# Kernel tuning notes

Hardware: AMD Instinct MI355X
Metric: run time of the kernel (lower is better)

Reference implementation:

```python
import jax, jax.numpy as jnp
import numpy as np

H = 1024
V = 5000
NUM_LAYERS = 2
B, T, U = 2, 128, 64


def setup_inputs() -> dict:
    key = jax.random.key(0)
    ks = jax.random.split(key, 16)
    s = 0.02
    inp = {
        "encoder_out": jax.random.normal(ks[0], (B, T, H), dtype=jnp.float32),
        "targets": jax.random.randint(ks[1], (B, U), 0, V),
        "embed": jax.random.normal(ks[2], (V, H), dtype=jnp.float32) * s,
        # stacked 2-layer LSTM params, PyTorch gate order (i, f, g, o)
        "lstm_Wih": jax.random.normal(ks[3], (NUM_LAYERS, 4 * H, H), dtype=jnp.float32) * s,
        "lstm_Whh": jax.random.normal(ks[4], (NUM_LAYERS, 4 * H, H), dtype=jnp.float32) * s,
        "lstm_bih": jnp.zeros((NUM_LAYERS, 4 * H), dtype=jnp.float32),
        "lstm_bhh": jnp.zeros((NUM_LAYERS, 4 * H), dtype=jnp.float32),
        "enc_W": jax.random.normal(ks[5], (H, H), dtype=jnp.float32) * s,
        "enc_b": jnp.zeros((H,), dtype=jnp.float32),
        "pred_W": jax.random.normal(ks[6], (H, H), dtype=jnp.float32) * s,
        "pred_b": jnp.zeros((H,), dtype=jnp.float32),
        "out_W": jax.random.normal(ks[7], (V + 1, H), dtype=jnp.float32) * s,
        "out_b": jnp.zeros((V + 1,), dtype=jnp.float32),
    }
    return inp


def _lstm_layer(x, Wih, Whh, bih, bhh):
    # x: [B, U, H] -> [B, U, H]; single LSTM layer, PyTorch gate order i,f,g,o
    b, u, h = x.shape
    bias = bih + bhh  # [4H]
    # precompute input projections for all timesteps: [U, B, 4H]
    xg = jnp.einsum('buh,gh->ubg', x, Wih) + bias

    def step(carry, xt):
        hprev, cprev = carry
        gates = xt + hprev @ Whh.T  # [B, 4H]
        i, f, g, o = jnp.split(gates, 4, axis=-1)
        i = jax.nn.sigmoid(i)
        f = jax.nn.sigmoid(f)
        g = jnp.tanh(g)
        o = jax.nn.sigmoid(o)
        c = f * cprev + i * g
        hnew = o * jnp.tanh(c)
        return (hnew, c), hnew

    init = (jnp.zeros((b, h), x.dtype), jnp.zeros((b, h), x.dtype))
    _, hs = jax.lax.scan(step, init, xg)  # hs: [U, B, H]
    return hs.transpose(1, 0, 2)


def reference(encoder_out, targets, embed, lstm_Wih, lstm_Whh, lstm_bih, lstm_bhh,
              enc_W, enc_b, pred_W, pred_b, out_W, out_b):
    # Prediction network: embedding + 2-layer LSTM (deterministic -> no dropout)
    x = embed[targets]  # [B, U, H]
    for l in range(NUM_LAYERS):
        x = _lstm_layer(x, lstm_Wih[l], lstm_Whh[l], lstm_bih[l], lstm_bhh[l])
    pred_out = x  # [B, U, H]

    # Joint network: proj + broadcast add over (T, U) + ReLU + output linear
    enc_p = jnp.einsum('bth,oh->bto', encoder_out, enc_W) + enc_b  # [B, T, H]
    prd_p = jnp.einsum('buh,oh->buo', pred_out, pred_W) + pred_b    # [B, U, H]
    joint = jax.nn.relu(enc_p[:, :, None, :] + prd_p[:, None, :, :])  # [B, T, U, H]
    logits = jnp.einsum('btuh,vh->btuv', joint, out_W) + out_b  # [B, T, U, V+1]
    return logits
```

## Files before the change

kernel.cpp:

```cpp
#include <hip/hip_runtime.h>
#include <hip/hip_bf16.h>

#define B_ 2
#define T_ 128
#define U_ 64
#define H_ 1024
#define NO_ 5001

typedef __attribute__((ext_vector_type(8))) short bf16x8;
typedef __attribute__((ext_vector_type(4))) float f32x4;
typedef __attribute__((ext_vector_type(4))) unsigned int uint4v;

__device__ __forceinline__ float bf2f(unsigned short s) {
  unsigned int u = ((unsigned int)s) << 16;
  float f; __builtin_memcpy(&f, &u, 4); return f;
}
__device__ __forceinline__ unsigned short f2bf(float f) {
  unsigned int u; __builtin_memcpy(&u, &f, 4);
  u = u + 0x7FFFu + ((u >> 16) & 1u);
  return (unsigned short)(u >> 16);
}
__device__ __forceinline__ float fsig(float x) {
  x = fminf(fmaxf(x, -30.f), 30.f);
  float e = __expf(-x);
  return __builtin_amdgcn_rcpf(1.f + e);
}
__device__ __forceinline__ float ftanh(float x) {
  x = fminf(fmaxf(x, -15.f), 15.f);
  float e = __expf(2.f * x);
  return (e - 1.f) * __builtin_amdgcn_rcpf(e + 1.f);
}

__device__ __forceinline__ void gload_lds16(const unsigned short* g, unsigned short* l) {
  __builtin_amdgcn_global_load_lds(
      (const __attribute__((address_space(1))) unsigned int*)g,
      (__attribute__((address_space(3))) unsigned int*)l,
      16, 0, 0);
}

#define R_OUTW 1280256
#define R_WIH  (R_OUTW + 2097152)
#define R_WHH  (R_WIH + 2097152)
#define R_ENCW (R_WHH + 262144)
#define R_PRDW (R_ENCW + 262144)
#define R_ENC  (R_PRDW + 65536)
#define R_BIAS (R_ENC + 1280)

__global__ void k_cvt_all(
    const float* __restrict__ outW, const float* __restrict__ Wih,
    const float* __restrict__ Whh,  const float* __restrict__ encW,
    const float* __restrict__ prdW, const float* __restrict__ enc,
    const float* __restrict__ outB,
    unsigned short* __restrict__ outW_bf, unsigned short* __restrict__ Wih_bf,
    unsigned short* __restrict__ Whh_bf,  unsigned short* __restrict__ encW_bf,
    unsigned short* __restrict__ prdW_bf, unsigned short* __restrict__ enc_bf,
    float* __restrict__ biasPad)
{
  int i = blockIdx.x * 256 + threadIdx.x;
  const float* src; unsigned short* dst; int off;
  if (i < R_OUTW)      { src = outW; dst = outW_bf; off = i; }
  else if (i < R_WIH)  { src = Wih;  dst = Wih_bf;  off = i - R_OUTW; }
  else if (i < R_WHH)  { src = Whh;  dst = Whh_bf;  off = i - R_WIH; }
  else if (i < R_ENCW) { src = encW; dst = encW_bf; off = i - R_WHH; }
  else if (i < R_PRDW) { src = prdW; dst = prdW_bf; off = i - R_ENCW; }
  else if (i < R_ENC)  { src = enc;  dst = enc_bf;  off = i - R_PRDW; }
  else {
    int e0 = (i - R_ENC) * 4;
    float4 v;
    v.x = (e0 + 0 < NO_) ? outB[e0 + 0] : 0.f;
    v.y = (e0 + 1 < NO_) ? outB[e0 + 1] : 0.f;
    v.z = (e0 + 2 < NO_) ? outB[e0 + 2] : 0.f;
    v.w = (e0 + 3 < NO_) ? outB[e0 + 3] : 0.f;
    *(float4*)&biasPad[e0] = v;
    return;
  }
  const float4 v = ((const float4*)src)[off];
  ushort4 o;
  o.x = f2bf(v.x); o.y = f2bf(v.y); o.z = f2bf(v.z); o.w = f2bf(v.w);
  ((ushort4*)dst)[off] = o;
}

__global__ void k_embed(const int* __restrict__ tg, const float* __restrict__ em,
                        unsigned short* __restrict__ x0) {
  int idx = blockIdx.x * 256 + threadIdx.x;
  int bu = idx >> 8;
  int kc = (idx & 255) << 2;
  int t = tg[bu];
  const float4 v = *(const float4*)&em[(long)t * H_ + kc];
  ushort4 o; o.x = f2bf(v.x); o.y = f2bf(v.y); o.z = f2bf(v.z); o.w = f2bf(v.w);
  *(ushort4*)&x0[bu * H_ + kc] = o;
}

__global__ __launch_bounds__(256) void gemm_bt(
    const unsigned short* __restrict__ A, const unsigned short* __restrict__ W,
    const float* __restrict__ b1, const float* __restrict__ b2,
    float* __restrict__ C, int M, int N, int K)
{
  __shared__ unsigned short As[128 * 32];
  __shared__ unsigned short Bs[128 * 32];
  const int tid = threadIdx.x;
  const int n0 = blockIdx.x * 128, m0 = blockIdx.y * 128;
  const int lane = tid & 63, w = tid >> 6;
  const int wr = (w >> 1) * 64, wc = (w & 1) * 64;
  const int lr = lane & 15, lk = (lane >> 4) * 8;
  f32x4 acc[4][4] = {};

  for (int k0 = 0; k0 < K; k0 += 32) {
#pragma unroll
    for (int s = 0; s < 2; ++s) {
      int idx = (w * 2 + s) * 64 + lane;
      int row = idx >> 2, c8 = (idx & 3) * 8;
      gload_lds16(&A[(long)(m0 + row) * K + k0 + c8], &As[(w * 2 + s) * 512]);
      gload_lds16(&W[(long)(n0 + row) * K + k0 + c8], &Bs[(w * 2 + s) * 512]);
    }
    __syncthreads();
    bf16x8 aF[4], bF[4];
#pragma unroll
    for (int i = 0; i < 4; ++i) {
      aF[i] = *(const bf16x8*)&As[(wr + i * 16 + lr) * 32 + lk];
      bF[i] = *(const bf16x8*)&Bs[(wc + i * 16 + lr) * 32 + lk];
    }
#pragma unroll
    for (int i = 0; i < 4; ++i)
#pragma unroll
      for (int j = 0; j < 4; ++j)
        acc[i][j] = __builtin_amdgcn_mfma_f32_16x16x32_bf16(aF[i], bF[j], acc[i][j], 0, 0, 0);
    __syncthreads();
  }

  const int lq = (lane >> 4) * 4;
#pragma unroll
  for (int j = 0; j < 4; ++j) {
    int col = n0 + wc + j * 16 + lr;
    if (col >= N) continue;
    float bb = 0.f;
    if (b1) bb += b1[col];
    if (b2) bb += b2[col];
#pragma unroll
    for (int i = 0; i < 4; ++i) {
      int rowg = m0 + wr + i * 16 + lq;
#pragma unroll
      for (int r = 0; r < 4; ++r)
        C[(long)(rowg + r) * N + col] = acc[i][j][r] + bb;
    }
  }
}

__global__ __launch_bounds__(256) void gemm_proj(
    const unsigned short* __restrict__ enc_bf, const unsigned short* __restrict__ x2_bf,
    const unsigned short* __restrict__ encW_bf, const unsigned short* __restrict__ prdW_bf,
    const float* __restrict__ encB, const float* __restrict__ prdB,
    float* __restrict__ ep, float* __restrict__ pp)
{
  __shared__ unsigned short As[128 * 32];
  __shared__ unsigned short Bs[128 * 32];
  const int tid = threadIdx.x;
  const unsigned short* A; const unsigned short* W; const float* b1; float* C;
  int m0;
  if (blockIdx.y < 2) { A = enc_bf; W = encW_bf; b1 = encB; C = ep; m0 = blockIdx.y * 128; }
  else                { A = x2_bf;  W = prdW_bf; b1 = prdB; C = pp; m0 = 0; }
  const int n0 = blockIdx.x * 128;
  const int K = H_, N = H_;
  const int lane = tid & 63, w = tid >> 6;
  const int wr = (w >> 1) * 64, wc = (w & 1) * 64;
  const int lr = lane & 15, lk = (lane >> 4) * 8;
  f32x4 acc[4][4] = {};

  for (int k0 = 0; k0 < K; k0 += 32) {
#pragma unroll
    for (int s = 0; s < 2; ++s) {
      int idx = (w * 2 + s) * 64 + lane;
      int row = idx >> 2, c8 = (idx & 3) * 8;
      gload_lds16(&A[(long)(m0 + row) * K + k0 + c8], &As[(w * 2 + s) * 512]);
      gload_lds16(&W[(long)(n0 + row) * K + k0 + c8], &Bs[(w * 2 + s) * 512]);
    }
    __syncthreads();
    bf16x8 aF[4], bF[4];
#pragma unroll
    for (int i = 0; i < 4; ++i) {
      aF[i] = *(const bf16x8*)&As[(wr + i * 16 + lr) * 32 + lk];
      bF[i] = *(const bf16x8*)&Bs[(wc + i * 16 + lr) * 32 + lk];
    }
#pragma unroll
    for (int i = 0; i < 4; ++i)
#pragma unroll
      for (int j = 0; j < 4; ++j)
        acc[i][j] = __builtin_amdgcn_mfma_f32_16x16x32_bf16(aF[i], bF[j], acc[i][j], 0, 0, 0);
    __syncthreads();
  }

  const int lq = (lane >> 4) * 4;
#pragma unroll
  for (int j = 0; j < 4; ++j) {
    int col = n0 + wc + j * 16 + lr;
    float bb = b1[col];
#pragma unroll
    for (int i = 0; i < 4; ++i) {
      int rowg = m0 + wr + i * 16 + lq;
#pragma unroll
      for (int r = 0; r < 4; ++r)
        C[(long)(rowg + r) * N + col] = acc[i][j][r] + bb;
    }
  }
}

#define STAGE_A(kt2, kh, rb) \
  gload_lds16(aSrc[rb] + (kt2) * 64 + (kh) * 32, \
              &As_f[((((kt2) & 1) * 2 + (kh)) * 8192) + ((rb) * 128 + wv * 16) * 32])
#define STAGE_B(kt2, kh, rb) \
  gload_lds16(bSrc[rb] + (kt2) * 64 + (kh) * 32, \
              &Bs_f[((((kt2) & 1) * 2 + (kh)) * 8192) + ((rb) * 128 + wv * 16) * 32])

__global__ __launch_bounds__(512, 1) void gemm_logits(
    const unsigned short* __restrict__ A, const unsigned short* __restrict__ W,
    const float* __restrict__ biasPad, float* __restrict__ C, int M, int N, int K)
{
  __shared__ __align__(16) unsigned short lds_all[65536];
  unsigned short* As_f = lds_all;
  unsigned short* Bs_f = lds_all + 32768;
  const int tid = threadIdx.x;
  const int lane = tid & 63, wv = tid >> 6;
  const int wm = wv >> 2, wn = wv & 3;
  int swzb = (blockIdx.x & 7) * 160 + (blockIdx.x >> 3);
  const int n0 = (swzb >> 6) * 256;
  const int m0 = (swzb & 63) * 256;
  const int NT = K / 64;

  const unsigned short* aSrc[2];
  const unsigned short* bSrc[2];
#pragma unroll
  for (int rb = 0; rb < 2; ++rb) {
    int rl = rb * 128 + (tid >> 2);
    int c2s = (tid & 3) ^ ((rl >> 1) & 3);
    aSrc[rb] = A + (long)(m0 + rl) * K + c2s * 8;
    bSrc[rb] = W + (long)(n0 + rl) * K + c2s * 8;
  }
  int aOff[8], bOff[4];
#pragma unroll
  for (int i = 0; i < 8; ++i) {
    int r = wm * 128 + i * 16 + (lane & 15);
    aOff[i] = r * 32 + (((lane >> 4) ^ ((r >> 1) & 3)) * 8);
  }
#pragma unroll
  for (int j = 0; j < 4; ++j) {
    int r = wn * 64 + j * 16 + (lane & 15);
    bOff[j] = r * 32 + (((lane >> 4) ^ ((r >> 1) & 3)) * 8);
  }

  f32x4 acc[8][4] = {};

  STAGE_A(0, 0, 0); STAGE_A(0, 0, 1); STAGE_B(0, 0, 0); STAGE_B(0, 0, 1);
  STAGE_A(0, 1, 0); STAGE_A(0, 1, 1); STAGE_B(0, 1, 0); STAGE_B(0, 1, 1);

  for (int kt = 0; kt < NT; ++kt) {
    const int b = kt & 1;
    asm volatile("s_waitcnt vmcnt(4)" ::: "memory");
    __builtin_amdgcn_s_barrier();
    __builtin_amdgcn_sched_barrier(0);
    {
      const int base = (b * 2 + 0) * 8192;
      bf16x8 aF[8], bF[4];
#pragma unroll
      for (int i = 0; i < 8; ++i) aF[i] = *(const bf16x8*)&As_f[base + aOff[i]];
#pragma unroll
      for (int j = 0; j < 4; ++j) bF[j] = *(const bf16x8*)&Bs_f[base + bOff[j]];
      if (kt + 1 < NT) {
        STAGE_A(kt + 1, 0, 0); STAGE_A(kt + 1, 0, 1);
        STAGE_B(kt + 1, 0, 0); STAGE_B(kt + 1, 0, 1);
        STAGE_A(kt + 1, 1, 0); STAGE_A(kt + 1, 1, 1);
      }
      __builtin_amdgcn_s_setprio(1);
#pragma unroll
      for (int i = 0; i < 8; ++i)
#pragma unroll
        for (int j = 0; j < 4; ++j)
          acc[i][j] = __builtin_amdgcn_mfma_f32_16x16x32_bf16(aF[i], bF[j], acc[i][j], 0, 0, 0);
      __builtin_amdgcn_s_setprio(0);
    }
    if (kt + 1 < NT) { asm volatile("s_waitcnt vmcnt(6)" ::: "memory"); }
    else             { asm volatile("s_waitcnt vmcnt(0)" ::: "memory"); }
    __builtin_amdgcn_s_barrier();
    __builtin_amdgcn_sched_barrier(0);
    {
      const int base = (b * 2 + 1) * 8192;
      bf16x8 aF[8], bF[4];
#pragma unroll
      for (int i = 0; i < 8; ++i) aF[i] = *(const bf16x8*)&As_f[base + aOff[i]];
#pragma unroll
      for (int j = 0; j < 4; ++j) bF[j] = *(const bf16x8*)&Bs_f[base + bOff[j]];
      if (kt + 1 < NT) { STAGE_B(kt + 1, 1, 0); STAGE_B(kt + 1, 1, 1); }
      __builtin_amdgcn_s_setprio(1);
#pragma unroll
      for (int i = 0; i < 8; ++i)
#pragma unroll
        for (int j = 0; j < 4; ++j)
          acc[i][j] = __builtin_amdgcn_mfma_f32_16x16x32_bf16(aF[i], bF[j], acc[i][j], 0, 0, 0);
      __builtin_amdgcn_s_setprio(0);
    }
  }

  float* eb = (float*)lds_all;
  const int lq = (lane >> 4) * 4;
  float bv4[4];
#pragma unroll
  for (int j = 0; j < 4; ++j) bv4[j] = biasPad[n0 + wn * 64 + j * 16 + (lane & 15)];

#pragma unroll
  for (int cp = 0; cp < 4; ++cp) {
    __syncthreads();
#pragma unroll
    for (int ii = 0; ii < 2; ++ii) {
      int rbase = wm * 32 + ii * 16 + lq;
#pragma unroll
      for (int j = 0; j < 4; ++j) {
        int col = wn * 64 + j * 16 + (lane & 15);
#pragma unroll
        for (int r = 0; r < 4; ++r)
          eb[(rbase + r) * 261 + col] = acc[cp * 2 + ii][j][r] + bv4[j];
      }
    }
    __syncthreads();
    {
      int rl = tid >> 3, ci = tid & 7;
      long grow = (long)m0 + (rl >> 5) * 128 + cp * 32 + (rl & 31);
      float* crow = C + grow * N + n0;
      const float* er = &eb[rl * 261];
#pragma unroll
      for (int k = 0; k < 8; ++k) {
        int col = ci * 4 + k * 32;
        float4 v = *(const float4*)&er[col];
        int gc = n0 + col;
        if (gc + 4 <= N) {
          *(float4*)&crow[col] = v;
        } else if (gc < N) {
          float tmp[4] = {v.x, v.y, v.z, v.w};
#pragma unroll
          for (int e = 0; e < 4; ++e)
            if (gc + e < N) crow[col + e] = tmp[e];
        }
      }
    }
  }
}

__global__ __launch_bounds__(256, 1) void lstm_fused3(
    const float* __restrict__ xg0,
    const unsigned short* __restrict__ Whh0,
    const unsigned short* __restrict__ Whh1,
    const unsigned short* __restrict__ Wih1,
    const float* __restrict__ bih1, const float* __restrict__ bhh1,
    unsigned short* __restrict__ x2_bf,
    float* __restrict__ hbuf0,
    float* __restrict__ hbuf1,
    float* __restrict__ xbuf,
    float* __restrict__ xgbuf,
    int*   __restrict__ flagsx)
{
  __shared__ float hs[2][H_];
  __shared__ float xgs[128][64];
  __shared__ float part[2][4][64][2];
  __shared__ float bias2s[64];

  const int tid = threadIdx.x;
  const int grp = blockIdx.x >> 6;
  const int bid = blockIdx.x & 63;
  const int w = tid >> 6, l = tid & 63;
  const int g = l >> 4, q = l & 15;
  const int row = g * 1024 + bid * 16 + q;
  const int kb = w * 256;

#define DOT_BODY(WREG, SRC)                                                              \
  _Pragma("unroll")                                                                      \
  for (int it = 0; it < 32; ++it) {                                                      \
    bf16x8 wv = WREG[it];                                                                \
    float4 h0a = *(const float4*)&SRC[0][kb + it * 8];                                   \
    float4 h0b = *(const float4*)&SRC[0][kb + it * 8 + 4];                               \
    float4 h1a = *(const float4*)&SRC[1][kb + it * 8];                                   \
    float4 h1b = *(const float4*)&SRC[1][kb + it * 8 + 4];                               \
    a00 += bf2f((unsigned short)wv[0]) * h0a.x + bf2f((unsigned short)wv[4]) * h0b.x;    \
    a01 += bf2f((unsigned short)wv[1]) * h0a.y + bf2f((unsigned short)wv[5]) * h0b.y;    \
    a02 += bf2f((unsigned short)wv[2]) * h0a.z + bf2f((unsigned short)wv[6]) * h0b.z;    \
    a03 += bf2f((unsigned short)wv[3]) * h0a.w + bf2f((unsigned short)wv[7]) * h0b.w;    \
    a10 += bf2f((unsigned short)wv[0]) * h1a.x + bf2f((unsigned short)wv[4]) * h1b.x;    \
    a11 += bf2f((unsigned short)wv[1]) * h1a.y + bf2f((unsigned short)wv[5]) * h1b.y;    \
    a12 += bf2f((unsigned short)wv[2]) * h1a.z + bf2f((unsigned short)wv[6]) * h1b.z;    \
    a13 += bf2f((unsigned short)wv[3]) * h1a.w + bf2f((unsigned short)wv[7]) * h1b.w;    \
  }

  if (grp == 0) {
    bf16x8 wreg[32];
#pragma unroll
    for (int it = 0; it < 32; ++it)
      wreg[it] = *(const bf16x8*)&Whh0[(long)row * H_ + kb + it * 8];
#pragma unroll
    for (int rep = 0; rep < 8; ++rep) {
      int c = rep * 256 + tid;
      int r2 = c >> 4, sub = c & 15;
      int gg = sub >> 2, f4 = sub & 3;
      const float4 v = *(const float4*)&xg0[(long)r2 * 4096 + gg * 1024 + bid * 16 + f4 * 4];
      *(float4*)&xgs[r2][gg * 16 + f4 * 4] = v;
    }
    __syncthreads();

    float creg = 0.f;
    for (int u = 0; u < U_; ++u) {
      const int p = u & 1;
      float a00 = 0.f, a01 = 0.f, a02 = 0.f, a03 = 0.f;
      float a10 = 0.f, a11 = 0.f, a12 = 0.f, a13 = 0.f;
      if (u > 0) {
        const float thr = 4.0f * u - 2.0f;
        const float* base = hbuf0 + (u & 1) * 2 * H_;
        const float* pa = base + tid * 4;
        const float* pb = base + H_ + tid * 4;
        float4 va, vb;
        for (;;) {
          asm volatile("global_load_dwordx4 %0, %2, off sc1\n\t"
                       "global_load_dwordx4 %1, %3, off sc1\n\t"
                       "s_waitcnt vmcnt(0)"
                       : "=v"(va), "=v"(vb) : "v"(pa), "v"(pb) : "memory");
          if (va.x > thr && va.y > thr && va.z > thr && va.w > thr &&
              vb.x > thr && vb.y > thr && vb.z > thr && vb.w > thr) break;
        }
        const float off = 4.0f * u;
        va.x -= off; va.y -= off; va.z -= off; va.w -= off;
        vb.x -= off; vb.y -= off; vb.z -= off; vb.w -= off;
        *(float4*)&hs[0][tid * 4] = va;
        *(float4*)&hs[1][tid * 4] = vb;
        DOT_BODY(wreg, hs)
      }
      part[p][w][l][0] = (a00 + a01) + (a02 + a03);
      part[p][w][l][1] = (a10 + a11) + (a12 + a13);
      __syncthreads();
      if (tid < 32) {
        int b = tid >> 4, qq = tid & 15;
        int bu = b * 64 + u;
        float gi = part[p][0][qq][b] + part[p][1][qq][b] + part[p][2][qq][b]
                 + part[p][3][qq][b] + xgs[bu][qq];
        float gf = part[p][0][16 + qq][b] + part[p][1][16 + qq][b] + part[p][2][16 + qq][b]
                 + part[p][3][16 + qq][b] + xgs[bu][16 + qq];
        float gc = part[p][0][32 + qq][b] + part[p][1][32 + qq][b] + part[p][2][32 + qq][b]
                 + part[p][3][32 + qq][b] + xgs[bu][32 + qq];
        float go = part[p][0][48 + qq][b] + part[p][1][48 + qq][b] + part[p][2][48 + qq][b]
                 + part[p][3][48 + qq][b] + xgs[bu][48 + qq];
        float i_ = fsig(gi), f_ = fsig(gf), g_ = ftanh(gc), o_ = fsig(go);
        creg = f_ * creg + i_ * g_;
        float h = o_ * ftanh(creg);
        int j = bid * 16 + qq;
        float tvx = h + 4.0f;
        const float* px = &xbuf[u * 2 * H_ + b * H_ + j];
        asm volatile("global_store_dword %0, %1, off sc1" :: "v"(px), "v"(tvx) : "memory");
        if (u < U_ - 1) {
          float tv = h + 4.0f * (u + 1);
          const float* pp2 = &hbuf0[((u + 1) & 1) * 2 * H_ + b * H_ + j];
          asm volatile("global_store_dword %0, %1, off sc1" :: "v"(pp2), "v"(tv) : "memory");
        }
      }
    }
  } else if (grp == 1) {
    bf16x8 wreg[32];
#pragma unroll
    for (int it = 0; it < 32; ++it)
      wreg[it] = *(const bf16x8*)&Wih1[(long)row * H_ + kb + it * 8];
    if (tid < 64) {
      int rr = (tid >> 4) * 1024 + bid * 16 + (tid & 15);
      bias2s[tid] = bih1[rr] + bhh1[rr];
    }
    __syncthreads();

    for (int u = 0; u < U_; ++u) {
      const int p = u & 1;
      const float* base = xbuf + u * 2 * H_;
      const float* pa = base + tid * 4;
      const float* pb = base + H_ + tid * 4;
      float4 va, vb;
      for (;;) {
        asm volatile("global_load_dwordx4 %0, %2, off sc1\n\t"
                     "global_load_dwordx4 %1, %3, off sc1\n\t"
                     "s_waitcnt vmcnt(0)"
                     : "=v"(va), "=v"(vb) : "v"(pa), "v"(pb) : "memory");
        if (va.x > 2.f && va.y > 2.f && va.z > 2.f && va.w > 2.f &&
            vb.x > 2.f && vb.y > 2.f && vb.z > 2.f && vb.w > 2.f) break;
        __builtin_amdgcn_s_sleep(2);
      }
      va.x -= 4.f; va.y -= 4.f; va.z -= 4.f; va.w -= 4.f;
      vb.x -= 4.f; vb.y -= 4.f; vb.z -= 4.f; vb.w -= 4.f;
      *(float4*)&hs[0][tid * 4] = va;
      *(float4*)&hs[1][tid * 4] = vb;

      float a00 = 0.f, a01 = 0.f, a02 = 0.f, a03 = 0.f;
      float a10 = 0.f, a11 = 0.f, a12 = 0.f, a13 = 0.f;
      DOT_BODY(wreg, hs)
      part[p][w][l][0] = (a00 + a01) + (a02 + a03);
      part[p][w][l][1] = (a10 + a11) + (a12 + a13);
      __syncthreads();
      if (tid < 128) {
        int b = tid >> 6, ll = tid & 63;
        float s = part[p][0][ll][b] + part[p][1][ll][b] + part[p][2][ll][b]
                + part[p][3][ll][b] + bias2s[ll];
        const float* pw = &xgbuf[((u * 64 + bid) * 2 + b) * 64 + ll];
        asm volatile("global_store_dword %0, %1, off sc1" :: "v"(pw), "v"(s) : "memory");
        asm volatile("s_waitcnt vmcnt(0)" ::: "memory");
      }
      __syncthreads();
      if (tid == 0) {
        int one = 1;
        const int* fp = &flagsx[(u * 64 + bid) * 16];
        asm volatile("global_store_dword %0, %1, off sc1" :: "v"(fp), "v"(one) : "memory");
      }
    }
  } else {
    bf16x8 wreg[32];
#pragma unroll
    for (int it = 0; it < 32; ++it)
      wreg[it] = *(const bf16x8*)&Whh1[(long)row * H_ + kb + it * 8];
    __syncthreads();

    float creg = 0.f;
    for (int u = 0; u < U_; ++u) {
      const int p = u & 1;
      {
        const int* fp = &flagsx[(u * 64 + bid) * 16];
        int fv;
        do {
          asm volatile("global_load_dword %0, %1, off sc1\n\ts_waitcnt vmcnt(0)"
                       : "=v"(fv) : "v"(fp) : "memory");
        } while (fv == 0);
      }
      float xgi = 0.f, xgf = 0.f, xgg = 0.f, xgo = 0.f;
      if (tid < 32) {
        int b = tid >> 4, qq = tid & 15;
        const float* xb = &xgbuf[((u * 64 + bid) * 2 + b) * 64];
        asm volatile("global_load_dword %0, %1, off sc1" : "=v"(xgi) : "v"(xb + qq) : "memory");
        asm volatile("global_load_dword %0, %1, off sc1" : "=v"(xgf) : "v"(xb + 16 + qq) : "memory");
        asm volatile("global_load_dword %0, %1, off sc1" : "=v"(xgg) : "v"(xb + 32 + qq) : "memory");
        asm volatile("global_load_dword %0, %1, off sc1" : "=v"(xgo) : "v"(xb + 48 + qq) : "memory");
        asm volatile("s_waitcnt vmcnt(0)" ::: "memory");
      }
      float a00 = 0.f, a01 = 0.f, a02 = 0.f, a03 = 0.f;
      float a10 = 0.f, a11 = 0.f, a12 = 0.f, a13 = 0.f;
      if (u > 0) {
        const float thr = 4.0f * u - 2.0f;
        const float* base = hbuf1 + (u & 1) * 2 * H_;
        const float* pa = base + tid * 4;
        const float* pb = base + H_ + tid * 4;
        float4 va, vb;
        for (;;) {
          asm volatile("global_load_dwordx4 %0, %2, off sc1\n\t"
                       "global_load_dwordx4 %1, %3, off sc1\n\t"
                       "s_waitcnt vmcnt(0)"
                       : "=v"(va), "=v"(vb) : "v"(pa), "v"(pb) : "memory");
          if (va.x > thr && va.y > thr && va.z > thr && va.w > thr &&
              vb.x > thr && vb.y > thr && vb.z > thr && vb.w > thr) break;
        }
        const float off = 4.0f * u;
        va.x -= off; va.y -= off; va.z -= off; va.w -= off;
        vb.x -= off; vb.y -= off; vb.z -= off; vb.w -= off;
        *(float4*)&hs[0][tid * 4] = va;
        *(float4*)&hs[1][tid * 4] = vb;
        DOT_BODY(wreg, hs)
      }
      part[p][w][l][0] = (a00 + a01) + (a02 + a03);
      part[p][w][l][1] = (a10 + a11) + (a12 + a13);
      __syncthreads();
      if (tid < 32) {
        int b = tid >> 4, qq = tid & 15;
        float gi = part[p][0][qq][b] + part[p][1][qq][b] + part[p][2][qq][b]
                 + part[p][3][qq][b] + xgi;
        float gf = part[p][0][16 + qq][b] + part[p][1][16 + qq][b] + part[p][2][16 + qq][b]
                 + part[p][3][16 + qq][b] + xgf;
        float gc = part[p][0][32 + qq][b] + part[p][1][32 + qq][b] + part[p][2][32 + qq][b]
                 + part[p][3][32 + qq][b] + xgg;
        float go = part[p][0][48 + qq][b] + part[p][1][48 + qq][b] + part[p][2][48 + qq][b]
                 + part[p][3][48 + qq][b] + xgo;
        float i_ = fsig(gi), f_ = fsig(gf), g_ = ftanh(gc), o_ = fsig(go);
        creg = f_ * creg + i_ * g_;
        float h = o_ * ftanh(creg);
        int j = bid * 16 + qq;
        x2_bf[(b * U_ + u) * H_ + j] = f2bf(h);
        if (u < U_ - 1) {
          float tv = h + 4.0f * (u + 1);
          const float* pp2 = &hbuf1[((u + 1) & 1) * 2 * H_ + b * H_ + j];
          asm volatile("global_store_dword %0, %1, off sc1" :: "v"(pp2), "v"(tv) : "memory");
        }
      }
    }
  }
#undef DOT_BODY
}

__global__ void k_joint(const float* __restrict__ ep, const float* __restrict__ pp,
                        unsigned short* __restrict__ jt)
{
  int idx = blockIdx.x * 256 + threadIdx.x;
  int m = idx >> 8;
  int kc = (idx & 255) << 2;
  int erow = m >> 6;
  int prow = (m >> 13) * U_ + (m & 63);
  const float4 e = *(const float4*)&ep[erow * H_ + kc];
  const float4 p = *(const float4*)&pp[prow * H_ + kc];
  float4 s;
  s.x = fmaxf(e.x + p.x, 0.f); s.y = fmaxf(e.y + p.y, 0.f);
  s.z = fmaxf(e.z + p.z, 0.f); s.w = fmaxf(e.w + p.w, 0.f);
  ushort4 o; o.x = f2bf(s.x); o.y = f2bf(s.y); o.z = f2bf(s.z); o.w = f2bf(s.w);
  *(ushort4*)&jt[m * H_ + kc] = o;
}

extern "C" void kernel_launch(void* const* d_in, const int* in_sizes, int n_in,
                              void* d_out, int out_size, void* d_ws, size_t ws_size,
                              hipStream_t stream)
{
  const float* enc   = (const float*)d_in[0];
  const int*   tg    = (const int*)d_in[1];
  const float* em    = (const float*)d_in[2];
  const float* Wih   = (const float*)d_in[3];
  const float* Whh   = (const float*)d_in[4];
  const float* bih   = (const float*)d_in[5];
  const float* bhh   = (const float*)d_in[6];
  const float* encW  = (const float*)d_in[7];
  const float* encB  = (const float*)d_in[8];
  const float* prdW  = (const float*)d_in[9];
  const float* prdB  = (const float*)d_in[10];
  const float* outW  = (const float*)d_in[11];
  const float* outB  = (const float*)d_in[12];
  float* out = (float*)d_out;
  char* ws = (char*)d_ws;

  unsigned short* outW_bf = (unsigned short*)(ws + 0);
  unsigned short* Wih_bf  = (unsigned short*)(ws + 10485760);
  unsigned short* Whh_bf  = (unsigned short*)(ws + 27262976);
  unsigned short* encW_bf = (unsigned short*)(ws + 44040192);
  unsigned short* prdW_bf = (unsigned short*)(ws + 46137344);
  unsigned short* enc_bf  = (unsigned short*)(ws + 48234496);
  unsigned short* x0_bf   = (unsigned short*)(ws + 48758784);
  unsigned short* x2_bf   = (unsigned short*)(ws + 49283072);
  float* xg  = (float*)(ws + 49545216);
  float* hbufL0 = (float*)(ws + 51642368);
  unsigned short* jt = (unsigned short*)(ws + 51659008);
  float* hbufL1 = (float*)(ws + 85213440);
  float* biasPad = (float*)(ws + 85229824);
  float* xbuf = (float*)(ws + 85250304);
  int* flagsx = (int*)(ws + 85774592);
  float* xgbuf = xg;
  float* ep = xg;
  float* pp = (float*)(ws + 49545216 + 1048576);

  hipMemsetAsync(hbufL0, 0, 16384, stream);
  hipMemsetAsync(hbufL1, 0, 86036736 - 85213440, stream);

  k_cvt_all<<<R_BIAS / 256, 256, 0, stream>>>(
      outW, Wih, Whh, encW, prdW, enc, outB,
      outW_bf, Wih_bf, Whh_bf, encW_bf, prdW_bf, enc_bf, biasPad);
  k_embed<<<(B_ * U_ * H_ / 4) / 256, 256, 0, stream>>>(tg, em, x0_bf);

  gemm_bt<<<dim3(32, 1), 256, 0, stream>>>(x0_bf, Wih_bf, bih, bhh, xg, B_ * U_, 4096, H_);
  lstm_fused3<<<192, 256, 0, stream>>>(xg, Whh_bf, Whh_bf + 4096 * H_, Wih_bf + 4096 * H_,
                                       bih + 4096, bhh + 4096, x2_bf,
                                       hbufL0, hbufL1, xbuf, xgbuf, flagsx);

  gemm_proj<<<dim3(8, 3), 256, 0, stream>>>(enc_bf, x2_bf, encW_bf, prdW_bf,
                                            encB, prdB, ep, pp);

  k_joint<<<16384, 256, 0, stream>>>(ep, pp, jt);
  gemm_logits<<<1280, 512, 0, stream>>>(jt, outW_bf, biasPad, out, B_ * T_ * U_, NO_, H_);
}
```

Baseline: 611.6 us.

## Fuse layer-0 input projection into persistent LSTM kernel as a producer group

Removes the separate gemm_bt launch that computed layer-0 input gate projections. The persistent LSTM kernel now runs four block groups instead of three: a new group computes layer-0 Wih·x per step and publishes each result behind a flag, and layer 0 and layer 1 recurrences share one code path that polls flags for their xg inputs. Spin loops gain s_sleep backoff. This trades a standalone GEMM and its full-size xg staging for more flag-based inter-block handshaking and 256 co-resident blocks, which must all be resident at once to avoid deadlock.

```diff
diff --git a/kernel.cpp b/kernel.cpp
--- a/kernel.cpp
+++ b/kernel.cpp
@@ -9,7 +9,6 @@
 
 typedef __attribute__((ext_vector_type(8))) short bf16x8;
 typedef __attribute__((ext_vector_type(4))) float f32x4;
-typedef __attribute__((ext_vector_type(4))) unsigned int uint4v;
 
 __device__ __forceinline__ float bf2f(unsigned short s) {
   unsigned int u = ((unsigned int)s) << 16;
@@ -91,61 +90,6 @@
   *(ushort4*)&x0[bu * H_ + kc] = o;
 }
 
-__global__ __launch_bounds__(256) void gemm_bt(
-    const unsigned short* __restrict__ A, const unsigned short* __restrict__ W,
-    const float* __restrict__ b1, const float* __restrict__ b2,
-    float* __restrict__ C, int M, int N, int K)
-{
-  __shared__ unsigned short As[128 * 32];
-  __shared__ unsigned short Bs[128 * 32];
-  const int tid = threadIdx.x;
-  const int n0 = blockIdx.x * 128, m0 = blockIdx.y * 128;
-  const int lane = tid & 63, w = tid >> 6;
-  const int wr = (w >> 1) * 64, wc = (w & 1) * 64;
-  const int lr = lane & 15, lk = (lane >> 4) * 8;
-  f32x4 acc[4][4] = {};
-
-  for (int k0 = 0; k0 < K; k0 += 32) {
-#pragma unroll
-    for (int s = 0; s < 2; ++s) {
-      int idx = (w * 2 + s) * 64 + lane;
-      int row = idx >> 2, c8 = (idx & 3) * 8;
-      gload_lds16(&A[(long)(m0 + row) * K + k0 + c8], &As[(w * 2 + s) * 512]);
-      gload_lds16(&W[(long)(n0 + row) * K + k0 + c8], &Bs[(w * 2 + s) * 512]);
-    }
-    __syncthreads();
-    bf16x8 aF[4], bF[4];
-#pragma unroll
-    for (int i = 0; i < 4; ++i) {
-      aF[i] = *(const bf16x8*)&As[(wr + i * 16 + lr) * 32 + lk];
-      bF[i] = *(const bf16x8*)&Bs[(wc + i * 16 + lr) * 32 + lk];
-    }
-#pragma unroll
-    for (int i = 0; i < 4; ++i)
-#pragma unroll
-      for (int j = 0; j < 4; ++j)
-        acc[i][j] = __builtin_amdgcn_mfma_f32_16x16x32_bf16(aF[i], bF[j], acc[i][j], 0, 0, 0);
-    __syncthreads();
-  }
-
-  const int lq = (lane >> 4) * 4;
-#pragma unroll
-  for (int j = 0; j < 4; ++j) {
-    int col = n0 + wc + j * 16 + lr;
-    if (col >= N) continue;
-    float bb = 0.f;
-    if (b1) bb += b1[col];
-    if (b2) bb += b2[col];
-#pragma unroll
-    for (int i = 0; i < 4; ++i) {
-      int rowg = m0 + wr + i * 16 + lq;
-#pragma unroll
-      for (int r = 0; r < 4; ++r)
-        C[(long)(rowg + r) * N + col] = acc[i][j][r] + bb;
-    }
-  }
-}
-
 __global__ __launch_bounds__(256) void gemm_proj(
     const unsigned short* __restrict__ enc_bf, const unsigned short* __restrict__ x2_bf,
     const unsigned short* __restrict__ encW_bf, const unsigned short* __restrict__ prdW_bf,
@@ -344,22 +288,23 @@
 }
 
 __global__ __launch_bounds__(256, 1) void lstm_fused3(
-    const float* __restrict__ xg0,
+    const unsigned short* __restrict__ x0_bf,
     const unsigned short* __restrict__ Whh0,
+    const unsigned short* __restrict__ Wih0,
     const unsigned short* __restrict__ Whh1,
     const unsigned short* __restrict__ Wih1,
+    const float* __restrict__ bih0, const float* __restrict__ bhh0,
     const float* __restrict__ bih1, const float* __restrict__ bhh1,
     unsigned short* __restrict__ x2_bf,
     float* __restrict__ hbuf0,
     float* __restrict__ hbuf1,
     float* __restrict__ xbuf,
-    float* __restrict__ xgbuf,
-    int*   __restrict__ flagsx)
+    float* __restrict__ xg1buf, int* __restrict__ flags1,
+    float* __restrict__ xg0buf, int* __restrict__ flags0)
 {
   __shared__ float hs[2][H_];
-  __shared__ float xgs[128][64];
   __shared__ float part[2][4][64][2];
-  __shared__ float bias2s[64];
+  __shared__ float biasS[64];
 
   const int tid = threadIdx.x;
   const int grp = blockIdx.x >> 6;
@@ -387,29 +332,42 @@
     a13 += bf2f((unsigned short)wv[3]) * h1a.w + bf2f((unsigned short)wv[7]) * h1b.w;    \
   }
 
-  if (grp == 0) {
+  if (grp == 0 || grp == 2) {
+    const unsigned short* Whh = (grp == 0) ? Whh0 : Whh1;
+    float* hbuf   = (grp == 0) ? hbuf0 : hbuf1;
+    const float* xgbufR = (grp == 0) ? xg0buf : xg1buf;
+    const int* flagsR   = (grp == 0) ? flags0 : flags1;
     bf16x8 wreg[32];
 #pragma unroll
     for (int it = 0; it < 32; ++it)
-      wreg[it] = *(const bf16x8*)&Whh0[(long)row * H_ + kb + it * 8];
-#pragma unroll
-    for (int rep = 0; rep < 8; ++rep) {
-      int c = rep * 256 + tid;
-      int r2 = c >> 4, sub = c & 15;
-      int gg = sub >> 2, f4 = sub & 3;
-      const float4 v = *(const float4*)&xg0[(long)r2 * 4096 + gg * 1024 + bid * 16 + f4 * 4];
-      *(float4*)&xgs[r2][gg * 16 + f4 * 4] = v;
-    }
+      wreg[it] = *(const bf16x8*)&Whh[(long)row * H_ + kb + it * 8];
     __syncthreads();
 
     float creg = 0.f;
     for (int u = 0; u < U_; ++u) {
       const int p = u & 1;
+      float xgi = 0.f, xgf = 0.f, xgg = 0.f, xgo = 0.f;
+      if (tid < 32) {
+        const int* fp = &flagsR[(u * 64 + bid) * 16];
+        int fv;
+        for (;;) {
+          asm volatile("global_load_dword %0, %1, off sc1\n\ts_waitcnt vmcnt(0)"
+                       : "=v"(fv) : "v"(fp) : "memory");
+          if (fv != 0) break;
+          __builtin_amdgcn_s_sleep(8);
+        }
+        const float* xb = &xgbufR[((u * 64 + bid) * 2 + (tid >> 4)) * 64];
+        int qq = tid & 15;
+        asm volatile("global_load_dword %0, %1, off sc1" : "=&v"(xgi) : "v"(xb + qq) : "memory");
+        asm volatile("global_load_dword %0, %1, off sc1" : "=&v"(xgf) : "v"(xb + 16 + qq) : "memory");
+        asm volatile("global_load_dword %0, %1, off sc1" : "=&v"(xgg) : "v"(xb + 32 + qq) : "memory");
+        asm volatile("global_load_dword %0, %1, off sc1" : "=&v"(xgo) : "v"(xb + 48 + qq) : "memory");
+      }
       float a00 = 0.f, a01 = 0.f, a02 = 0.f, a03 = 0.f;
       float a10 = 0.f, a11 = 0.f, a12 = 0.f, a13 = 0.f;
       if (u > 0) {
         const float thr = 4.0f * u - 2.0f;
-        const float* base = hbuf0 + (u & 1) * 2 * H_;
+        const float* base = hbuf + (u & 1) * 2 * H_;
         const float* pa = base + tid * 4;
         const float* pb = base + H_ + tid * 4;
         float4 va, vb;
@@ -420,6 +378,7 @@
                        : "=v"(va), "=v"(vb) : "v"(pa), "v"(pb) : "memory");
           if (va.x > thr && va.y > thr && va.z > thr && va.w > thr &&
               vb.x > thr && vb.y > thr && vb.z > thr && vb.w > thr) break;
+          __builtin_amdgcn_s_sleep(8);
         }
         const float off = 4.0f * u;
         va.x -= off; va.y -= off; va.z -= off; va.w -= off;
@@ -430,137 +389,10 @@
       }
       part[p][w][l][0] = (a00 + a01) + (a02 + a03);
       part[p][w][l][1] = (a10 + a11) + (a12 + a13);
-      __syncthreads();
       if (tid < 32) {
-        int b = tid >> 4, qq = tid & 15;
-        int bu = b * 64 + u;
-        float gi = part[p][0][qq][b] + part[p][1][qq][b] + part[p][2][qq][b]
-                 + part[p][3][qq][b] + xgs[bu][qq];
-        float gf = part[p][0][16 + qq][b] + part[p][1][16 + qq][b] + part[p][2][16 + qq][b]
-                 + part[p][3][16 + qq][b] + xgs[bu][16 + qq];
-        float gc = part[p][0][32 + qq][b] + part[p][1][32 + qq][b] + part[p][2][32 + qq][b]
-                 + part[p][3][32 + qq][b] + xgs[bu][32 + qq];
-        float go = part[p][0][48 + qq][b] + part[p][1][48 + qq][b] + part[p][2][48 + qq][b]
-                 + part[p][3][48 + qq][b] + xgs[bu][48 + qq];
-        float i_ = fsig(gi), f_ = fsig(gf), g_ = ftanh(gc), o_ = fsig(go);
-        creg = f_ * creg + i_ * g_;
-        float h = o_ * ftanh(creg);
-        int j = bid * 16 + qq;
-        float tvx = h + 4.0f;
-        const float* px = &xbuf[u * 2 * H_ + b * H_ + j];
-        asm volatile("global_store_dword %0, %1, off sc1" :: "v"(px), "v"(tvx) : "memory");
-        if (u < U_ - 1) {
-          float tv = h + 4.0f * (u + 1);
-          const float* pp2 = &hbuf0[((u + 1) & 1) * 2 * H_ + b * H_ + j];
-          asm volatile("global_store_dword %0, %1, off sc1" :: "v"(pp2), "v"(tv) : "memory");
-        }
-      }
-    }
-  } else if (grp == 1) {
-    bf16x8 wreg[32];
-#pragma unroll
-    for (int it = 0; it < 32; ++it)
-      wreg[it] = *(const bf16x8*)&Wih1[(long)row * H_ + kb + it * 8];
-    if (tid < 64) {
-      int rr = (tid >> 4) * 1024 + bid * 16 + (tid & 15);
-      bias2s[tid] = bih1[rr] + bhh1[rr];
-    }
-    __syncthreads();
-
-    for (int u = 0; u < U_; ++u) {
-      const int p = u & 1;
-      const float* base = xbuf + u * 2 * H_;
-      const float* pa = base + tid * 4;
-      const float* pb = base + H_ + tid * 4;
-      float4 va, vb;
-      for (;;) {
-        asm volatile("global_load_dwordx4 %0, %2, off sc1\n\t"
-                     "global_load_dwordx4 %1, %3, off sc1\n\t"
-                     "s_waitcnt vmcnt(0)"
-                     : "=v"(va), "=v"(vb) : "v"(pa), "v"(pb) : "memory");
-        if (va.x > 2.f && va.y > 2.f && va.z > 2.f && va.w > 2.f &&
-            vb.x > 2.f && vb.y > 2.f && vb.z > 2.f && vb.w > 2.f) break;
-        __builtin_amdgcn_s_sleep(2);
-      }
-      va.x -= 4.f; va.y -= 4.f; va.z -= 4.f; va.w -= 4.f;
-      vb.x -= 4.f; vb.y -= 4.f; vb.z -= 4.f; vb.w -= 4.f;
-      *(float4*)&hs[0][tid * 4] = va;
-      *(float4*)&hs[1][tid * 4] = vb;
-
-      float a00 = 0.f, a01 = 0.f, a02 = 0.f, a03 = 0.f;
-      float a10 = 0.f, a11 = 0.f, a12 = 0.f, a13 = 0.f;
-      DOT_BODY(wreg, hs)
-      part[p][w][l][0] = (a00 + a01) + (a02 + a03);
-      part[p][w][l][1] = (a10 + a11) + (a12 + a13);
-      __syncthreads();
-      if (tid < 128) {
-        int b = tid >> 6, ll = tid & 63;
-        float s = part[p][0][ll][b] + part[p][1][ll][b] + part[p][2][ll][b]
-                + part[p][3][ll][b] + bias2s[ll];
-        const float* pw = &xgbuf[((u * 64 + bid) * 2 + b) * 64 + ll];
-        asm volatile("global_store_dword %0, %1, off sc1" :: "v"(pw), "v"(s) : "memory");
-        asm volatile("s_waitcnt vmcnt(0)" ::: "memory");
-      }
-      __syncthreads();
-      if (tid == 0) {
-        int one = 1;
-        const int* fp = &flagsx[(u * 64 + bid) * 16];
-        asm volatile("global_store_dword %0, %1, off sc1" :: "v"(fp), "v"(one) : "memory");
-      }
-    }
-  } else {
-    bf16x8 wreg[32];
-#pragma unroll
-    for (int it = 0; it < 32; ++it)
-      wreg[it] = *(const bf16x8*)&Whh1[(long)row * H_ + kb + it * 8];
-    __syncthreads();
-
-    float creg = 0.f;
-    for (int u = 0; u < U_; ++u) {
-      const int p = u & 1;
-      {
-        const int* fp = &flagsx[(u * 64 + bid) * 16];
-        int fv;
-        do {
-          asm volatile("global_load_dword %0, %1, off sc1\n\ts_waitcnt vmcnt(0)"
-                       : "=v"(fv) : "v"(fp) : "memory");
-        } while (fv == 0);
-      }
-      float xgi = 0.f, xgf = 0.f, xgg = 0.f, xgo = 0.f;
-      if (tid < 32) {
-        int b = tid >> 4, qq = tid & 15;
-        const float* xb = &xgbuf[((u * 64 + bid) * 2 + b) * 64];
-        asm volatile("global_load_dword %0, %1, off sc1" : "=v"(xgi) : "v"(xb + qq) : "memory");
-        asm volatile("global_load_dword %0, %1, off sc1" : "=v"(xgf) : "v"(xb + 16 + qq) : "memory");
-        asm volatile("global_load_dword %0, %1, off sc1" : "=v"(xgg) : "v"(xb + 32 + qq) : "memory");
-        asm volatile("global_load_dword %0, %1, off sc1" : "=v"(xgo) : "v"(xb + 48 + qq) : "memory");
-        asm volatile("s_waitcnt vmcnt(0)" ::: "memory");
-      }
-      float a00 = 0.f, a01 = 0.f, a02 = 0.f, a03 = 0.f;
-      float a10 = 0.f, a11 = 0.f, a12 = 0.f, a13 = 0.f;
-      if (u > 0) {
-        const float thr = 4.0f * u - 2.0f;
-        const float* base = hbuf1 + (u & 1) * 2 * H_;
-        const float* pa = base + tid * 4;
-        const float* pb = base + H_ + tid * 4;
-        float4 va, vb;
-        for (;;) {
-          asm volatile("global_load_dwordx4 %0, %2, off sc1\n\t"
-                       "global_load_dwordx4 %1, %3, off sc1\n\t"
-                       "s_waitcnt vmcnt(0)"
-                       : "=v"(va), "=v"(vb) : "v"(pa), "v"(pb) : "memory");
-          if (va.x > thr && va.y > thr && va.z > thr && va.w > thr &&
-              vb.x > thr && vb.y > thr && vb.z > thr && vb.w > thr) break;
-        }
-        const float off = 4.0f * u;
-        va.x -= off; va.y -= off; va.z -= off; va.w -= off;
-        vb.x -= off; vb.y -= off; vb.z -= off; vb.w -= off;
-        *(float4*)&hs[0][tid * 4] = va;
-        *(float4*)&hs[1][tid * 4] = vb;
-        DOT_BODY(wreg, hs)
-      }
-      part[p][w][l][0] = (a00 + a01) + (a02 + a03);
-      part[p][w][l][1] = (a10 + a11) + (a12 + a13);
+        asm volatile("s_waitcnt vmcnt(0)"
+                     : "+v"(xgi), "+v"(xgf), "+v"(xgg), "+v"(xgo) :: "memory");
+      }
       __syncthreads();
       if (tid < 32) {
         int b = tid >> 4, qq = tid & 15;
@@ -576,12 +408,86 @@
         creg = f_ * creg + i_ * g_;
         float h = o_ * ftanh(creg);
         int j = bid * 16 + qq;
-        x2_bf[(b * U_ + u) * H_ + j] = f2bf(h);
+        if (grp == 0) {
+          float tvx = h + 4.0f;
+          const float* px = &xbuf[u * 2 * H_ + b * H_ + j];
+          asm volatile("global_store_dword %0, %1, off sc1" :: "v"(px), "v"(tvx) : "memory");
+        } else {
+          x2_bf[(b * U_ + u) * H_ + j] = f2bf(h);
+        }
         if (u < U_ - 1) {
           float tv = h + 4.0f * (u + 1);
-          const float* pp2 = &hbuf1[((u + 1) & 1) * 2 * H_ + b * H_ + j];
+          const float* pp2 = &hbuf[((u + 1) & 1) * 2 * H_ + b * H_ + j];
           asm volatile("global_store_dword %0, %1, off sc1" :: "v"(pp2), "v"(tv) : "memory");
         }
+      }
+    }
+  } else {
+    const bool isX1 = (grp == 1);
+    const unsigned short* Wih = isX1 ? Wih1 : Wih0;
+    const float* bihp = isX1 ? bih1 : bih0;
+    const float* bhhp = isX1 ? bhh1 : bhh0;
+    float* xgbufW = isX1 ? xg1buf : xg0buf;
+    int* flagsW   = isX1 ? flags1 : flags0;
+    bf16x8 wreg[32];
+#pragma unroll
+    for (int it = 0; it < 32; ++it)
+      wreg[it] = *(const bf16x8*)&Wih[(long)row * H_ + kb + it * 8];
+    if (tid < 64) {
+      int rr = (tid >> 4) * 1024 + bid * 16 + (tid & 15);
+      biasS[tid] = bihp[rr] + bhhp[rr];
+    }
+    __syncthreads();
+
+    for (int u = 0; u < U_; ++u) {
+      const int p = u & 1;
+      if (isX1) {
+        const float* base = xbuf + u * 2 * H_;
+        const float* pa = base + tid * 4;
+        const float* pb = base + H_ + tid * 4;
+        float4 va, vb;
+        for (;;) {
+          asm volatile("global_load_dwordx4 %0, %2, off sc1\n\t"
+                       "global_load_dwordx4 %1, %3, off sc1\n\t"
+                       "s_waitcnt vmcnt(0)"
+                       : "=v"(va), "=v"(vb) : "v"(pa), "v"(pb) : "memory");
+          if (va.x > 2.f && va.y > 2.f && va.z > 2.f && va.w > 2.f &&
+              vb.x > 2.f && vb.y > 2.f && vb.z > 2.f && vb.w > 2.f) break;
+          __builtin_amdgcn_s_sleep(8);
+        }
+        va.x -= 4.f; va.y -= 4.f; va.z -= 4.f; va.w -= 4.f;
+        vb.x -= 4.f; vb.y -= 4.f; vb.z -= 4.f; vb.w -= 4.f;
+        *(float4*)&hs[0][tid * 4] = va;
+        *(float4*)&hs[1][tid * 4] = vb;
+      } else {
+        ushort4 xa = *(const ushort4*)&x0_bf[(0 * U_ + u) * H_ + tid * 4];
+        ushort4 xb = *(const ushort4*)&x0_bf[(1 * U_ + u) * H_ + tid * 4];
+        float4 va, vb;
+        va.x = bf2f(xa.x); va.y = bf2f(xa.y); va.z = bf2f(xa.z); va.w = bf2f(xa.w);
+        vb.x = bf2f(xb.x); vb.y = bf2f(xb.y); vb.z = bf2f(xb.z); vb.w = bf2f(xb.w);
+        *(float4*)&hs[0][tid * 4] = va;
+        *(float4*)&hs[1][tid * 4] = vb;
+      }
+
+      float a00 = 0.f, a01 = 0.f, a02 = 0.f, a03 = 0.f;
+      float a10 = 0.f, a11 = 0.f, a12 = 0.f, a13 = 0.f;
+      DOT_BODY(wreg, hs)
+      part[p][w][l][0] = (a00 + a01) + (a02 + a03);
+      part[p][w][l][1] = (a10 + a11) + (a12 + a13);
+      __syncthreads();
+      if (tid < 128) {
+        int b = tid >> 6, ll = tid & 63;
+        float s = part[p][0][ll][b] + part[p][1][ll][b] + part[p][2][ll][b]
+                + part[p][3][ll][b] + biasS[ll];
+        const float* pw = &xgbufW[((u * 64 + bid) * 2 + b) * 64 + ll];
+        asm volatile("global_store_dword %0, %1, off sc1" :: "v"(pw), "v"(s) : "memory");
+        asm volatile("s_waitcnt vmcnt(0)" ::: "memory");
+      }
+      __syncthreads();
+      if (tid == 0) {
+        int one = 1;
+        const int* fp = &flagsW[(u * 64 + bid) * 16];
+        asm volatile("global_store_dword %0, %1, off sc1" :: "v"(fp), "v"(one) : "memory");
       }
     }
   }
@@ -633,29 +539,34 @@
   unsigned short* enc_bf  = (unsigned short*)(ws + 48234496);
   unsigned short* x0_bf   = (unsigned short*)(ws + 48758784);
   unsigned short* x2_bf   = (unsigned short*)(ws + 49283072);
-  float* xg  = (float*)(ws + 49545216);
+  float* xg1buf = (float*)(ws + 49545216);
   float* hbufL0 = (float*)(ws + 51642368);
   unsigned short* jt = (unsigned short*)(ws + 51659008);
+  int*   flags0 = (int*)(ws + 51659008);
+  float* xg0buf = (float*)(ws + 51659008 + 262144);
   float* hbufL1 = (float*)(ws + 85213440);
   float* biasPad = (float*)(ws + 85229824);
   float* xbuf = (float*)(ws + 85250304);
-  int* flagsx = (int*)(ws + 85774592);
-  float* xgbuf = xg;
-  float* ep = xg;
+  int* flags1 = (int*)(ws + 85774592);
+  float* ep = (float*)(ws + 49545216);
   float* pp = (float*)(ws + 49545216 + 1048576);
 
   hipMemsetAsync(hbufL0, 0, 16384, stream);
   hipMemsetAsync(hbufL1, 0, 86036736 - 85213440, stream);
+  hipMemsetAsync(flags0, 0, 262144, stream);
 
   k_cvt_all<<<R_BIAS / 256, 256, 0, stream>>>(
       outW, Wih, Whh, encW, prdW, enc, outB,
       outW_bf, Wih_bf, Whh_bf, encW_bf, prdW_bf, enc_bf, biasPad);
   k_embed<<<(B_ * U_ * H_ / 4) / 256, 256, 0, stream>>>(tg, em, x0_bf);
 
-  gemm_bt<<<dim3(32, 1), 256, 0, stream>>>(x0_bf, Wih_bf, bih, bhh, xg, B_ * U_, 4096, H_);
-  lstm_fused3<<<192, 256, 0, stream>>>(xg, Whh_bf, Whh_bf + 4096 * H_, Wih_bf + 4096 * H_,
-                                       bih + 4096, bhh + 4096, x2_bf,
-                                       hbufL0, hbufL1, xbuf, xgbuf, flagsx);
+  lstm_fused3<<<256, 256, 0, stream>>>(
+      x0_bf,
+      Whh_bf, Wih_bf,
+      Whh_bf + 4096 * H_, Wih_bf + 4096 * H_,
+      bih, bhh, bih + 4096, bhh + 4096,
+      x2_bf, hbufL0, hbufL1, xbuf,
+      xg1buf, flags1, xg0buf, flags0);
 
   gemm_proj<<<dim3(8, 3), 256, 0, stream>>>(enc_bf, x2_bf, encW_bf, prdW_bf,
                                             encB, prdB, ep, pp);
```

Result: faster. 599.5 us (-2.0%).
